# Kernel optimization log

Hardware: AMD Instinct MI355X
Metric: run time of the kernel (lower is better)

## Reference

```python
import math
import jax, jax.numpy as jnp
import numpy as np

NUM_HEADS = 16
NUM_LANDMARKS = 64
INV_ITERS = 6
ATT_SIZE = 1024
HEAD_SIZE = ATT_SIZE // NUM_HEADS  # dk = 64
NEG = -100000.0


def moore_penrose_pinv(x, num_iter):
    # lucidrains-style iterative Moore-Penrose pseudo-inverse
    abs_x = jnp.abs(x)
    col = abs_x.sum(axis=-1)
    row = abs_x.sum(axis=-2)
    z = jnp.swapaxes(x, -1, -2) / (jnp.max(col) * jnp.max(row))
    I = jnp.eye(x.shape[-1], dtype=x.dtype)
    for _ in range(num_iter):
        xz = x @ z
        z = 0.25 * z @ (13.0 * I - xz @ (15.0 * I - xz @ (7.0 * I - xz)))
    return z


def masked_softmax_scores(k, q, mask):
    # q @ k^T (dk=1: q already scaled) + mask, softmax over last dim
    s = jnp.einsum('bhmd,bhld->bhml', q, k)
    if mask is not None:
        s = s + (1.0 - mask) * NEG
    return jax.nn.softmax(s, axis=-1)


def setup_inputs() -> dict:
    key = jax.random.key(0)
    k1, k2, k3 = jax.random.split(key, 3)
    B, L, D = 4, 4096, 1024
    x = jax.random.normal(k1, (B, L, D), dtype=jnp.float32)
    attention_mask = jnp.ones((B, L), dtype=jnp.float32)
    w_kqv = jax.random.normal(k2, (3 * ATT_SIZE, D), dtype=jnp.float32) * 0.02
    w_out = jax.random.normal(k3, (ATT_SIZE, ATT_SIZE), dtype=jnp.float32) * 0.02
    b_out = jnp.zeros((ATT_SIZE,), dtype=jnp.float32)
    return {"x": x, "attention_mask": attention_mask,
            "w_kqv": w_kqv, "w_out": w_out, "b_out": b_out}


def reference(x, attention_mask, w_kqv, w_out, b_out):
    B, L, D = x.shape
    H, nl, hd = NUM_HEADS, NUM_LANDMARKS, HEAD_SIZE
    seg = L // nl  # landmark segment length (L already a multiple of nl)

    kqv = x @ w_kqv.T  # [B, L, 3A]
    k, q, v = jnp.split(kqv, 3, axis=-1)
    split = lambda t: t.reshape(B, L, H, hd).transpose(0, 2, 1, 3)  # [B,H,L,hd]
    k, q, v = split(k), split(q), split(v)

    mask = attention_mask[:, None, :]  # [B,1,L]
    denom = mask.reshape(B, 1, nl, seg).sum(-1) + 1e-08  # [B,1,nl]
    mask_lm = (denom > 0).astype(x.dtype)  # [B,1,nl]
    denom4 = denom[..., None]              # [B,1,nl,1]
    maskL = mask[..., None]                # [B,1,L,1]

    q = q * maskL
    k = k * maskL
    v = v * maskL

    s1_mask = maskL * mask_lm[..., None, :]               # [B,1,L,nl]
    s2_mask = mask_lm[..., None] * mask_lm[..., None, :]  # [B,1,nl,nl]
    s3_mask = jnp.swapaxes(s1_mask, -1, -2)               # [B,1,nl,L]

    q = q / math.sqrt(HEAD_SIZE)
    q_lm = q.reshape(B, H, nl, seg, hd).sum(-2) / denom4  # [B,H,nl,hd]
    k_lm = k.reshape(B, H, nl, seg, hd).sum(-2) / denom4

    scores_1 = masked_softmax_scores(k_lm, q, s1_mask)     # [B,H,L,nl]
    scores_2 = masked_softmax_scores(k_lm, q_lm, s2_mask)  # [B,H,nl,nl]
    scores_3 = masked_softmax_scores(k, q_lm, s3_mask)     # [B,H,nl,L]

    z_star = moore_penrose_pinv(scores_2, INV_ITERS)       # [B,H,nl,nl]
    out = scores_1 @ (z_star @ (scores_3 @ v))             # [B,H,L,hd]

    out = out.transpose(0, 2, 1, 3).reshape(B, L, H * hd)  # merge heads
    return out @ w_out.T + b_out
```

## Files before the change

kernel.cpp:

```cpp
#include <hip/hip_runtime.h>
#include <hip/hip_bf16.h>


static constexpr int Bn  = 4;
static constexpr int Ln  = 4096;
static constexpr int Dn  = 1024;
static constexpr int Hn  = 16;
static constexpr int HDn = 64;
static constexpr int NLn = 64;
static constexpr int SEGn = 64;
static constexpr int BHn = Bn * Hn;
static constexpr int Mn  = Bn * Ln;
static constexpr int NCH = 8;
#define NEG_BIG (-100000.0f)

static constexpr size_t OFF_KT  = 0;
static constexpr size_t OFF_QT  = 16777216;
static constexpr size_t OFF_VT  = 33554432;
static constexpr size_t OFF_WOH = 33554432;
static constexpr size_t OFF_WH  = 50331648;
static constexpr size_t OFF_QLM = 50331648;
static constexpr size_t OFF_KLM = 50593792;
static constexpr size_t OFF_S2  = 50855936;
static constexpr size_t OFF_Z   = 51118080;
static constexpr size_t OFF_WM  = 51380224;
static constexpr size_t OFF_PM  = 51642368;
static constexpr size_t OFF_PS  = 51675136;
static constexpr size_t OFF_GM  = 51707904;
static constexpr size_t OFF_XS  = 53477376;
static constexpr size_t OFF_PO  = 53477376;

using bf16x8 = __attribute__((ext_vector_type(8))) short;
using f32x16 = __attribute__((ext_vector_type(16))) float;
using s16x4  = __attribute__((ext_vector_type(4))) short;

__device__ __forceinline__ unsigned short f2bf(float f) {
    unsigned int u = __float_as_uint(f);
    return (unsigned short)((u + 0x7fffu + ((u >> 16) & 1u)) >> 16);
}
__device__ __forceinline__ void cvt8r(const float* fs, bf16x8& hv) {
    #pragma unroll
    for (int e = 0; e < 8; ++e) hv[e] = (short)f2bf(fs[e]);
}
typedef __attribute__((address_space(1))) void gvoid;
typedef __attribute__((address_space(3))) void lvoid;
__device__ __forceinline__ void async16(void* l, const void* g) {
    __builtin_amdgcn_global_load_lds((gvoid*)(size_t)g, (lvoid*)l, 16, 0, 0);
}

__global__ __launch_bounds__(256) void k_pack(
    const float* __restrict__ src, unsigned short* __restrict__ dh, int row0)
{
    __shared__ float Ls[128][33];
    const int rt = blockIdx.x, kt = blockIdx.y;
    const int tid = threadIdx.x;
    #pragma unroll
    for (int p = 0; p < 4; ++p) {
        const int row = p * 32 + (tid >> 3);
        const int c4 = (tid & 7) * 4;
        const float4 v = *(const float4*)&src[(size_t)(row0 + rt * 128 + row) * 1024 + kt * 32 + c4];
        Ls[row][c4 + 0] = v.x; Ls[row][c4 + 1] = v.y;
        Ls[row][c4 + 2] = v.z; Ls[row][c4 + 3] = v.w;
    }
    __syncthreads();
    const size_t tb = (size_t)(rt * 32 + kt) * 4096;
    for (int s = tid; s < 512; s += 256) {
        const int g = s >> 7, kk = (s >> 6) & 1, l = s & 63;
        const int row = g * 32 + (l & 31);
        const int k0 = kk * 16 + ((l >> 5) & 1) * 8;
        bf16x8 hv;
        cvt8r(&Ls[row][k0], hv);
        *(bf16x8*)&dh[tb + s * 8] = hv;
    }
}

#define GEMM4W_CORE(A_, B_, NNB)                                               \
    __shared__ __attribute__((aligned(16))) char smem[16384];                  \
    const int tid = threadIdx.x;                                               \
    const int lane = tid & 63, wid = tid >> 6;                                 \
    const int cpx = gridDim.x >> 3;                                            \
    const int wg = (blockIdx.x & 7) * cpx + (blockIdx.x >> 3);                 \
    const int bm = wg / (NNB), bn = wg % (NNB);                                \
    const int wrow = wid >> 1, wcol = wid & 1;                                 \
    const unsigned short* gsrc =                                               \
        (wid < 2 ? (A_) + (size_t)bm * 131072 : (B_) + (size_t)bn * 131072)    \
        + (wid & 1) * 2048 + lane * 8;                                         \
    char* ldst = smem + wid * 4096;                                            \
    f32x16 acc[2][2] = {};                                                     \
    for (int kt = 0; kt < 32; ++kt) {                                          \
        const unsigned short* g = gsrc + (size_t)kt * 4096;                    \
        __syncthreads();                                                       \
        _Pragma("unroll")                                                      \
        for (int i = 0; i < 4; ++i)                                            \
            async16(ldst + i * 1024, g + i * 512);                             \
        __syncthreads();                                                       \
        _Pragma("unroll")                                                      \
        for (int kk = 0; kk < 2; ++kk) {                                       \
            bf16x8 fa[2], fb[2];                                               \
            _Pragma("unroll")                                                  \
            for (int ti = 0; ti < 2; ++ti) {                                   \
                const int o = (((wrow * 2 + ti) * 2 + kk) << 10) + lane * 16;  \
                fa[ti] = *(const bf16x8*)(smem + o);                           \
            }                                                                  \
            _Pragma("unroll")                                                  \
            for (int tj = 0; tj < 2; ++tj) {                                   \
                const int o = (((wcol * 2 + tj) * 2 + kk) << 10) + lane * 16;  \
                fb[tj] = *(const bf16x8*)(smem + 8192 + o);                    \
            }                                                                  \
            _Pragma("unroll")                                                  \
            for (int ti = 0; ti < 2; ++ti)                                     \
                _Pragma("unroll")                                              \
                for (int tj = 0; tj < 2; ++tj)                                 \
                    acc[ti][tj] = __builtin_amdgcn_mfma_f32_32x32x16_bf16(     \
                        fa[ti], fb[tj], acc[ti][tj], 0, 0, 0);                 \
        }                                                                      \
    }

__global__ __launch_bounds__(256) void k_kqv_gemm(
    const unsigned short* __restrict__ xh,
    const unsigned short* __restrict__ wh,
    const float* __restrict__ mask,
    float* __restrict__ Kt, float* __restrict__ Qt, float* __restrict__ Vt,
    int row0)
{
    GEMM4W_CORE(xh, wh, 24)
    const int part = bn >> 3;
    #pragma unroll
    for (int ti = 0; ti < 2; ++ti) {
        #pragma unroll
        for (int tj = 0; tj < 2; ++tj) {
            const int col = (bn * 128 + wcol * 64 + tj * 32 + (lane & 31)) & 1023;
            const int h = col >> 6, d = col & 63;
            #pragma unroll
            for (int r = 0; r < 16; ++r) {
                const int row = row0 + bm * 128 + wrow * 64 + ti * 32
                              + (r & 3) + 8 * (r >> 2) + 4 * (lane >> 5);
                const int b = row >> 12, l = row & 4095;
                const float mk = mask[b * Ln + l];
                const size_t idx = ((size_t)(b * Hn + h) * Ln + l) * HDn + d;
                const float v = acc[ti][tj][r] * mk;
                if (part == 0)      Kt[idx] = v;
                else if (part == 1) Qt[idx] = v * 0.125f;
                else                Vt[idx] = v;
            }
        }
    }
}

__global__ __launch_bounds__(256) void k_out_gemm(
    const unsigned short* __restrict__ ah_,
    const unsigned short* __restrict__ bh_,
    const float* __restrict__ bias, float* __restrict__ out)
{
    GEMM4W_CORE(ah_, bh_, 8)
    #pragma unroll
    for (int ti = 0; ti < 2; ++ti) {
        #pragma unroll
        for (int tj = 0; tj < 2; ++tj) {
            const int col = bn * 128 + wcol * 64 + tj * 32 + (lane & 31);
            const float bb = bias[col];
            #pragma unroll
            for (int r = 0; r < 16; ++r) {
                const int row = bm * 128 + wrow * 64 + ti * 32
                              + (r & 3) + 8 * (r >> 2) + 4 * (lane >> 5);
                out[(size_t)row * Dn + col] = acc[ti][tj][r] + bb;
            }
        }
    }
}

__global__ __launch_bounds__(64) void k_landmarks(
    const float* __restrict__ Kt, const float* __restrict__ Qt,
    const float* __restrict__ mask,
    float* __restrict__ klm, float* __restrict__ qlm, int* __restrict__ gmax)
{
    const int blk = blockIdx.x;
    const int m = blk & 63, bh = blk >> 6, b = bh >> 4;
    const int d = threadIdx.x;
    if (blk == 0 && d < 2) gmax[d] = 0;
    float mv = mask[b * Ln + m * SEGn + d];
    #pragma unroll
    for (int off = 32; off; off >>= 1) mv += __shfl_down(mv, off);
    const float denom = __shfl(mv, 0) + 1e-8f;
    const float* kp = Kt + ((size_t)bh * Ln + m * SEGn) * HDn + d;
    const float* qp = Qt + ((size_t)bh * Ln + m * SEGn) * HDn + d;
    float sk = 0.f, sq = 0.f;
    for (int j = 0; j < SEGn; ++j) {
        sk += kp[(size_t)j * HDn];
        sq += qp[(size_t)j * HDn];
    }
    klm[((size_t)bh * NLn + m) * HDn + d] = sk / denom;
    qlm[((size_t)bh * NLn + m) * HDn + d] = sq / denom;
}

__global__ __launch_bounds__(256) void k_s2(
    const float* __restrict__ qlm, const float* __restrict__ klm,
    float* __restrict__ s2, int* __restrict__ gmax)
{
    const int bh = blockIdx.x;
    __shared__ float ql[64][65];
    __shared__ float kl[64][65];
    __shared__ float sr[64][65];
    __shared__ float red[64][4], red2[64][4];
    __shared__ float rtmp[64], ctmp[64];
    const int tid = threadIdx.x;
    for (int idx = tid; idx < 4096; idx += 256) {
        ql[idx >> 6][idx & 63] = qlm[(size_t)bh * 4096 + idx];
        kl[idx >> 6][idx & 63] = klm[(size_t)bh * 4096 + idx];
    }
    __syncthreads();
    const int row = tid >> 2, sg = tid & 3, c0 = sg * 16;
    float sv[16];
    float mx = -1e30f;
    #pragma unroll 4
    for (int m = 0; m < 16; ++m) {
        float s = 0.f;
        #pragma unroll 8
        for (int d2 = 0; d2 < 64; ++d2) s = fmaf(ql[row][d2], kl[c0 + m][d2], s);
        sv[m] = s;
        mx = fmaxf(mx, s);
    }
    red[row][sg] = mx;
    __syncthreads();
    mx = fmaxf(fmaxf(red[row][0], red[row][1]), fmaxf(red[row][2], red[row][3]));
    float sum = 0.f;
    #pragma unroll
    for (int m = 0; m < 16; ++m) {
        const float e = __expf(sv[m] - mx);
        sv[m] = e;
        sum += e;
    }
    red2[row][sg] = sum;
    __syncthreads();
    const float inv = 1.f / (red2[row][0] + red2[row][1] + red2[row][2] + red2[row][3]);
    float rs = 0.f;
    #pragma unroll
    for (int m = 0; m < 16; ++m) {
        const float v = sv[m] * inv;
        sr[row][c0 + m] = v;
        s2[(size_t)bh * 4096 + row * 64 + c0 + m] = v;
        rs += fabsf(v);
    }
    red[row][sg] = rs;
    __syncthreads();
    if (sg == 0)
        rtmp[row] = red[row][0] + red[row][1] + red[row][2] + red[row][3];
    float cs = 0.f;
    #pragma unroll
    for (int r = 0; r < 16; ++r) cs += fabsf(sr[c0 + r][row]);
    red2[row][sg] = cs;
    __syncthreads();
    if (sg == 0)
        ctmp[row] = red2[row][0] + red2[row][1] + red2[row][2] + red2[row][3];
    __syncthreads();
    if (tid < 64) {
        float rmax = rtmp[tid], cmax = ctmp[tid];
        #pragma unroll
        for (int off = 32; off; off >>= 1) {
            rmax = fmaxf(rmax, __shfl_down(rmax, off));
            cmax = fmaxf(cmax, __shfl_down(cmax, off));
        }
        if (tid == 0) {
            atomicMax(&gmax[0], __float_as_int(rmax));
            atomicMax(&gmax[1], __float_as_int(cmax));
        }
    }
}

template<int SUB>
__device__ __forceinline__ void mm64v(
    float* C, int ldc, const float* Ag, int lda,
    const float* Bm, int ldb, float dg, float scl)
{
    const int tid = threadIdx.x;
    const int tx = tid & 15, ty = tid >> 4;
    const int i0 = ty << 2, j0 = tx << 2;
    float acc[4][4] = {};
    for (int k0 = 0; k0 < 64; k0 += 4) {
        float4 a4[4], b4[4];
        #pragma unroll
        for (int i = 0; i < 4; ++i)
            a4[i] = *(const float4*)&Ag[(size_t)(i0 + i) * lda + k0];
        #pragma unroll
        for (int kk = 0; kk < 4; ++kk)
            b4[kk] = *(const float4*)&Bm[(size_t)(k0 + kk) * ldb + j0];
        if (SUB) {
            #pragma unroll
            for (int kk = 0; kk < 4; ++kk) {
                float* bp = (float*)&b4[kk];
                #pragma unroll
                for (int j = 0; j < 4; ++j)
                    bp[j] = ((k0 + kk == j0 + j) ? dg : 0.0f) - bp[j];
            }
        }
        #pragma unroll
        for (int i = 0; i < 4; ++i) {
            const float* ap = (const float*)&a4[i];
            #pragma unroll
            for (int kk = 0; kk < 4; ++kk) {
                const float* bp = (const float*)&b4[kk];
                #pragma unroll
                for (int j = 0; j < 4; ++j)
                    acc[i][j] = fmaf(ap[kk], bp[j], acc[i][j]);
            }
        }
    }
    __syncthreads();
    #pragma unroll
    for (int i = 0; i < 4; ++i)
        #pragma unroll
        for (int j = 0; j < 4; ++j) C[(size_t)(i0 + i) * ldc + j0 + j] = scl * acc[i][j];
    __syncthreads();
}

__global__ __launch_bounds__(256) void k_pinv_s3v(
    const float* __restrict__ s2, const int* __restrict__ gmax,
    float* __restrict__ zout,
    const float* __restrict__ qlm, const float* __restrict__ Kt,
    const float* __restrict__ Vt, const float* __restrict__ mask,
    float* __restrict__ Opart, float* __restrict__ mpart, float* __restrict__ spart)
{
    __shared__ __attribute__((aligned(16))) char shm[61184];
    const int tid = threadIdx.x;

    if (blockIdx.y == NCH) {
        float (*Zb)[68] = (float(*)[68])(shm);
        float (*XZ)[68] = (float(*)[68])(shm + 17408);
        float (*Tb)[68] = (float(*)[68])(shm + 34816);
        const int bh = blockIdx.x;
        const float* X = s2 + (size_t)bh * 4096;
        const float scale = 1.0f / (__int_as_float(gmax[0]) * __int_as_float(gmax[1]));
        for (int idx = tid; idx < 4096; idx += 256) {
            const int i = idx >> 6, j = idx & 63;
            Zb[i][j] = X[j * 64 + i] * scale;
        }
        __syncthreads();
        for (int it = 0; it < 6; ++it) {
            mm64v<0>(&XZ[0][0], 68, X, 64, &Zb[0][0], 68, 0.f, 1.f);
            mm64v<1>(&Tb[0][0], 68, &XZ[0][0], 68, &XZ[0][0], 68, 7.f, 1.f);
            mm64v<1>(&Tb[0][0], 68, &XZ[0][0], 68, &Tb[0][0], 68, 15.f, 1.f);
            mm64v<1>(&Zb[0][0], 68, &Zb[0][0], 68, &Tb[0][0], 68, 13.f, 0.25f);
        }
        for (int idx = tid; idx < 4096; idx += 256)
            zout[(size_t)bh * 4096 + idx] = Zb[idx >> 6][idx & 63];
        return;
    }

    float (*Sm)[65] = (float(*)[65])(shm);
    float (*Ks)[65] = (float(*)[65])(shm + 16640);
    float (*Vs)[65] = (float(*)[65])(shm + 33280);
    unsigned short* Qp = (unsigned short*)(shm + 49920);
    float (*red)[4]  = (float(*)[4])(shm + 58112);
    float (*red2)[4] = (float(*)[4])(shm + 59136);
    float* rowmax = (float*)(shm + 60160);
    float* rowsum = (float*)(shm + 60416);
    float* fac    = (float*)(shm + 60672);
    float* mrow   = (float*)(shm + 60928);
    const int bh = blockIdx.x, ch = blockIdx.y;
    const int b = bh >> 4;
    const int lane = tid & 63, wid = tid >> 6;
    const int wr = wid >> 1, wc = wid & 1;

    for (int idx = tid; idx < 4096; idx += 256)
        Sm[idx >> 6][idx & 63] = qlm[(size_t)bh * 4096 + idx];
    if (tid < 64) { rowmax[tid] = -1e30f; rowsum[tid] = 0.f; }
    __syncthreads();
    for (int s = tid; s < 512; s += 256) {
        const int g = s >> 8, kc = (s >> 6) & 3, l = s & 63;
        const int row = g * 32 + (l & 31);
        const int k0 = kc * 16 + ((l >> 5) & 1) * 8;
        bf16x8 hv;
        cvt8r(&Sm[row][k0], hv);
        *(bf16x8*)&Qp[s * 8] = hv;
    }
    f32x16 accO = {};
    const int t0beg = ch * (Ln / NCH), t0end = t0beg + (Ln / NCH);
    for (int t0 = t0beg; t0 < t0end; t0 += 64) {
        __syncthreads();
        for (int idx = tid; idx < 4096; idx += 256) {
            const int r = idx >> 6, c2 = idx & 63;
            Ks[r][c2] = Kt[((size_t)bh * Ln + t0 + r) * HDn + c2];
            Vs[r][c2] = Vt[((size_t)bh * Ln + t0 + r) * HDn + c2];
        }
        if (tid < 64) mrow[tid] = mask[b * Ln + t0 + tid];
        __syncthreads();
        f32x16 acc = {};
        #pragma unroll
        for (int kc = 0; kc < 4; ++kc) {
            const bf16x8 a_h = *(const bf16x8*)&Qp[((wr * 4 + kc) * 64 + lane) * 8];
            const int brow = wc * 32 + (lane & 31);
            const int k0 = kc * 16 + (lane >> 5) * 8;
            bf16x8 b_h;
            cvt8r(&Ks[brow][k0], b_h);
            acc = __builtin_amdgcn_mfma_f32_32x32x16_bf16(a_h, b_h, acc, 0, 0, 0);
        }
        #pragma unroll
        for (int r = 0; r < 16; ++r) {
            const int row = wr * 32 + (r & 3) + 8 * (r >> 2) + 4 * (lane >> 5);
            const int col = wc * 32 + (lane & 31);
            Sm[row][col] = acc[r] + (1.f - mrow[col]) * NEG_BIG;
        }
        __syncthreads();
        {
            const int row = tid >> 2, sg = tid & 3, c0 = sg * 16;
            float mx = -1e30f;
            #pragma unroll
            for (int c = 0; c < 16; ++c) mx = fmaxf(mx, Sm[row][c0 + c]);
            red[row][sg] = mx;
            __syncthreads();
            const float nm = fmaxf(rowmax[row],
                fmaxf(fmaxf(red[row][0], red[row][1]), fmaxf(red[row][2], red[row][3])));
            const float f = __expf(rowmax[row] - nm);
            float ps = 0.f;
            #pragma unroll
            for (int c = 0; c < 16; ++c) {
                const float e = __expf(Sm[row][c0 + c] - nm);
                Sm[row][c0 + c] = e;
                ps += e;
            }
            red2[row][sg] = ps;
            __syncthreads();
            if (sg == 0) {
                rowsum[row] = rowsum[row] * f
                    + red2[row][0] + red2[row][1] + red2[row][2] + red2[row][3];
                rowmax[row] = nm;
                fac[row] = f;
            }
        }
        __syncthreads();
        #pragma unroll
        for (int r = 0; r < 16; ++r) {
            const int row = wr * 32 + (r & 3) + 8 * (r >> 2) + 4 * (lane >> 5);
            accO[r] *= fac[row];
        }
        #pragma unroll
        for (int kc = 0; kc < 4; ++kc) {
            const int arow = wr * 32 + (lane & 31);
            const int ak0 = kc * 16 + (lane >> 5) * 8;
            bf16x8 a_h;
            cvt8r(&Sm[arow][ak0], a_h);
            const int bcol = wc * 32 + (lane & 31);
            const int bk0 = kc * 16 + (lane >> 5) * 8;
            float bw[8];
            #pragma unroll
            for (int e = 0; e < 8; ++e) bw[e] = Vs[bk0 + e][bcol];
            bf16x8 b_h;
            cvt8r(bw, b_h);
            accO = __builtin_amdgcn_mfma_f32_32x32x16_bf16(a_h, b_h, accO, 0, 0, 0);
        }
    }
    __syncthreads();
    #pragma unroll
    for (int r = 0; r < 16; ++r) {
        const int row = wr * 32 + (r & 3) + 8 * (r >> 2) + 4 * (lane >> 5);
        Vs[row][wc * 32 + (lane & 31)] = accO[r];
    }
    __syncthreads();
    const size_t ob = (size_t)(bh * NCH + ch) * 4096;
    for (int idx = tid; idx < 4096; idx += 256)
        Opart[ob + idx] = Vs[idx >> 6][idx & 63];
    if (tid < 64) {
        mpart[(bh * NCH + ch) * 64 + tid] = rowmax[tid];
        spart[(bh * NCH + ch) * 64 + tid] = rowsum[tid];
    }
}

__global__ __launch_bounds__(256) void k_mergez(
    const float* __restrict__ Opart, const float* __restrict__ mpart,
    const float* __restrict__ spart, const float* __restrict__ Zs,
    float* __restrict__ Wm)
{
    __shared__ float Sv[64][68];
    __shared__ float Zb[64][68];
    const int bh = blockIdx.x, tid = threadIdx.x;
    for (int idx = tid; idx < 4096; idx += 256)
        Zb[idx >> 6][idx & 63] = Zs[(size_t)bh * 4096 + idx];
    {
        const int r = tid >> 2, c0 = (tid & 3) * 16;
        float e[NCH];
        float M = -1e30f;
        #pragma unroll
        for (int c = 0; c < NCH; ++c) {
            e[c] = mpart[(bh * NCH + c) * 64 + r];
            M = fmaxf(M, e[c]);
        }
        float S = 0.f;
        #pragma unroll
        for (int c = 0; c < NCH; ++c) {
            e[c] = expf(e[c] - M);
            S += spart[(bh * NCH + c) * 64 + r] * e[c];
        }
        const float invS = 1.f / S;
        for (int col = c0; col < c0 + 16; ++col) {
            float o = 0.f;
            #pragma unroll
            for (int c = 0; c < NCH; ++c)
                o += Opart[(size_t)(bh * NCH + c) * 4096 + r * 64 + col] * e[c];
            Sv[r][col] = o * invS;
        }
    }
    __syncthreads();
    const int tx = tid & 15, ty = tid >> 4;
    const int i0 = ty << 2, j0 = tx << 2;
    float acc[4][4] = {};
    for (int k0 = 0; k0 < 64; k0 += 4) {
        float4 a4[4], b4[4];
        #pragma unroll
        for (int i = 0; i < 4; ++i)
            a4[i] = *(const float4*)&Zb[i0 + i][k0];
        #pragma unroll
        for (int kk = 0; kk < 4; ++kk)
            b4[kk] = *(const float4*)&Sv[k0 + kk][j0];
        #pragma unroll
        for (int i = 0; i < 4; ++i) {
            const float* ap = (const float*)&a4[i];
            #pragma unroll
            for (int kk = 0; kk < 4; ++kk) {
                const float* bp = (const float*)&b4[kk];
                #pragma unroll
                for (int j = 0; j < 4; ++j)
                    acc[i][j] = fmaf(ap[kk], bp[j], acc[i][j]);
            }
        }
    }
    #pragma unroll
    for (int i = 0; i < 4; ++i)
        #pragma unroll
        for (int j = 0; j < 4; ++j)
            Wm[(size_t)bh * 4096 + (i0 + i) * 64 + j0 + j] = acc[i][j];
}

__global__ __launch_bounds__(256) void k_attn_out(
    const float* __restrict__ Qt, const float* __restrict__ klm,
    const float* __restrict__ Wm, unsigned short* __restrict__ ah)
{
    const int lt0 = blockIdx.x * 4;
    const int bh = blockIdx.y;
    const int b = bh >> 4, h = bh & 15;
    __shared__ float Sm[64][65];
    __shared__ float Ks[64][65];
    __shared__ float Ws[64][65];
    __shared__ float Ob[64][65];
    __shared__ unsigned short Qp[4096];
    __shared__ float red[64][4], red2[64][4];
    __shared__ float invr[64];
    const int tid = threadIdx.x;
    const int lane = tid & 63, wid = tid >> 6;
    const int wr = wid >> 1, wc = wid & 1;

    for (int idx = tid; idx < 4096; idx += 256) {
        const int r = idx >> 6, c2 = idx & 63;
        Ks[r][c2] = klm[(size_t)bh * 4096 + idx];
        Ws[r][c2] = Wm[(size_t)bh * 4096 + idx];
    }
    __syncthreads();

    for (int sub = 0; sub < 4; ++sub) {
        const int lt = lt0 + sub;
        for (int idx = tid; idx < 4096; idx += 256)
            Sm[idx >> 6][idx & 63] = Qt[((size_t)bh * Ln + lt * 64 + (idx >> 6)) * HDn + (idx & 63)];
        __syncthreads();
        for (int s = tid; s < 512; s += 256) {
            const int g = s >> 8, kc = (s >> 6) & 3, l = s & 63;
            const int row = g * 32 + (l & 31);
            const int k0 = kc * 16 + ((l >> 5) & 1) * 8;
            bf16x8 hv;
            cvt8r(&Sm[row][k0], hv);
            *(bf16x8*)&Qp[s * 8] = hv;
        }
        __syncthreads();
        f32x16 acc = {};
        #pragma unroll
        for (int kc = 0; kc < 4; ++kc) {
            const bf16x8 a_h = *(const bf16x8*)&Qp[((wr * 4 + kc) * 64 + lane) * 8];
            const int brow = wc * 32 + (lane & 31);
            const int k0 = kc * 16 + (lane >> 5) * 8;
            bf16x8 b_h;
            cvt8r(&Ks[brow][k0], b_h);
            acc = __builtin_amdgcn_mfma_f32_32x32x16_bf16(a_h, b_h, acc, 0, 0, 0);
        }
        #pragma unroll
        for (int r = 0; r < 16; ++r) {
            const int row = wr * 32 + (r & 3) + 8 * (r >> 2) + 4 * (lane >> 5);
            Sm[row][wc * 32 + (lane & 31)] = acc[r];
        }
        __syncthreads();
        {
            const int row = tid >> 2, sg = tid & 3, c0 = sg * 16;
            float mx = -1e30f;
            #pragma unroll
            for (int c = 0; c < 16; ++c) mx = fmaxf(mx, Sm[row][c0 + c]);
            red[row][sg] = mx;
            __syncthreads();
            mx = fmaxf(fmaxf(red[row][0], red[row][1]), fmaxf(red[row][2], red[row][3]));
            float ps = 0.f;
            #pragma unroll
            for (int c = 0; c < 16; ++c) {
                const float e = __expf(Sm[row][c0 + c] - mx);
                Sm[row][c0 + c] = e;
                ps += e;
            }
            red2[row][sg] = ps;
            __syncthreads();
            if (sg == 0)
                invr[row] = 1.f / (red2[row][0] + red2[row][1] + red2[row][2] + red2[row][3]);
        }
        __syncthreads();
        f32x16 acc2 = {};
        #pragma unroll
        for (int kc = 0; kc < 4; ++kc) {
            const int arow = wr * 32 + (lane & 31);
            const int ak0 = kc * 16 + (lane >> 5) * 8;
            bf16x8 a_h;
            cvt8r(&Sm[arow][ak0], a_h);
            const int bcol = wc * 32 + (lane & 31);
            const int bk0 = kc * 16 + (lane >> 5) * 8;
            float bw[8];
            #pragma unroll
            for (int e = 0; e < 8; ++e) bw[e] = Ws[bk0 + e][bcol];
            bf16x8 b_h;
            cvt8r(bw, b_h);
            acc2 = __builtin_amdgcn_mfma_f32_32x32x16_bf16(a_h, b_h, acc2, 0, 0, 0);
        }
        __syncthreads();
        #pragma unroll
        for (int r = 0; r < 16; ++r) {
            const int row = wr * 32 + (r & 3) + 8 * (r >> 2) + 4 * (lane >> 5);
            Ob[row][wc * 32 + (lane & 31)] = acc2[r];
        }
        __syncthreads();
        {
            const int tx = tid & 15, ty = tid >> 4;
            const int i0 = ty << 2, j0 = tx << 2;
            const int kd = h * 64 + j0;
            const int kt2 = kd >> 5, kc2 = kd & 31;
            const int kk2 = kc2 >> 4, half = (kc2 & 15) >> 3, e0 = kc2 & 7;
            #pragma unroll
            for (int i = 0; i < 4; ++i) {
                const float inv = invr[i0 + i];
                const int gm = b * Ln + lt * 64 + i0 + i;
                const int mt = gm >> 7, g2 = (gm & 127) >> 5, lrow = gm & 31;
                const size_t u = (size_t)(mt * 32 + kt2) * 4096
                               + (size_t)(((g2 * 2 + kk2) * 64 + half * 32 + lrow) * 8 + e0);
                s16x4 hv;
                #pragma unroll
                for (int j = 0; j < 4; ++j)
                    hv[j] = (short)f2bf(Ob[i0 + i][j0 + j] * inv);
                *(s16x4*)&ah[u] = hv;
            }
        }
        __syncthreads();
    }
}

extern "C" void kernel_launch(void* const* d_in, const int* in_sizes, int n_in,
                              void* d_out, int out_size, void* d_ws, size_t ws_size,
                              hipStream_t stream)
{
    (void)in_sizes; (void)n_in; (void)out_size;
    const float* x    = (const float*)d_in[0];
    const float* mask = (const float*)d_in[1];
    const float* wkqv = (const float*)d_in[2];
    const float* wout = (const float*)d_in[3];
    const float* bout = (const float*)d_in[4];
    float* out = (float*)d_out;
    float* ws  = (float*)d_ws;

    float* Kt   = ws + OFF_KT;
    float* Qt   = ws + OFF_QT;
    float* Vt   = ws + OFF_VT;
    float* qlm  = ws + OFF_QLM;
    float* klm  = ws + OFF_KLM;
    float* s2   = ws + OFF_S2;
    float* zst  = ws + OFF_Z;
    float* Wm   = ws + OFF_WM;
    int*   gmax = (int*)(ws + OFF_GM);
    float* mpart = ws + OFF_PM;
    float* spart = ws + OFF_PS;
    float* Opart = ws + OFF_PO;
    unsigned short* wh  = (unsigned short*)(ws + OFF_WH);
    unsigned short* woh = (unsigned short*)(ws + OFF_WOH);
    unsigned short* attn_h = (unsigned short*)(ws + OFF_KT);

    int S = 2048;
    if (ws_size >= (size_t)(OFF_XS + 16384 * 512) * 4) S = 16384;
    else if (ws_size >= (size_t)(OFF_XS + 8192 * 512) * 4) S = 8192;
    else if (ws_size >= (size_t)(OFF_XS + 2097152) * 4) S = 4096;
    unsigned short* xhs = (unsigned short*)(ws + OFF_XS);

    k_pack<<<dim3(24, 32), 256, 0, stream>>>(wkqv, wh, 0);
    for (int s = 0; s < Mn / S; ++s) {
        k_pack<<<dim3(S / 128, 32), 256, 0, stream>>>(x, xhs, s * S);
        k_kqv_gemm<<<(S / 128) * 24, 256, 0, stream>>>(
            xhs, wh, mask, Kt, Qt, Vt, s * S);
    }
    k_landmarks<<<BHn * NLn, 64, 0, stream>>>(Kt, Qt, mask, klm, qlm, gmax);
    k_s2<<<BHn, 256, 0, stream>>>(qlm, klm, s2, gmax);
    k_pinv_s3v<<<dim3(BHn, NCH + 1), 256, 0, stream>>>(
        s2, gmax, zst, qlm, Kt, Vt, mask, Opart, mpart, spart);
    k_pack<<<dim3(8, 32), 256, 0, stream>>>(wout, woh, 0);
    k_mergez<<<BHn, 256, 0, stream>>>(Opart, mpart, spart, zst, Wm);
    k_attn_out<<<dim3(Ln / 256, BHn), 256, 0, stream>>>(Qt, klm, Wm, attn_h);
    k_out_gemm<<<128 * 8, 256, 0, stream>>>(attn_h, woh, bout, out);
}
```

Baseline: 402.5 us.

## Double-buffer LDS tiles in GEMM core with async prefetch two stages ahead

Splits the shared-memory staging buffer of the 4-wave GEMM core into two halves. The async global-to-LDS loads for chunks c+1 and c+2 are issued while chunk c is being computed, with explicit vmcnt waits and raw s_barrier calls replacing the two __syncthreads per iteration. The goal is to hide global load latency behind the MFMA work in the QKV and output projection GEMMs. In exchange it doubles LDS use per block, which may reduce occupancy, and the hand-written waitcnt logic depends on each wave having exactly four outstanding loads per chunk.

```diff
diff --git a/kernel.cpp b/kernel.cpp
--- a/kernel.cpp
+++ b/kernel.cpp
@@ -75,7 +75,7 @@
 }
 
 #define GEMM4W_CORE(A_, B_, NNB)                                               \
-    __shared__ __attribute__((aligned(16))) char smem[16384];                  \
+    __shared__ __attribute__((aligned(16))) char smem[2][16384];               \
     const int tid = threadIdx.x;                                               \
     const int lane = tid & 63, wid = tid >> 6;                                 \
     const int cpx = gridDim.x >> 3;                                            \
@@ -85,34 +85,47 @@
     const unsigned short* gsrc =                                               \
         (wid < 2 ? (A_) + (size_t)bm * 131072 : (B_) + (size_t)bn * 131072)    \
         + (wid & 1) * 2048 + lane * 8;                                         \
-    char* ldst = smem + wid * 4096;                                            \
     f32x16 acc[2][2] = {};                                                     \
-    for (int kt = 0; kt < 32; ++kt) {                                          \
-        const unsigned short* g = gsrc + (size_t)kt * 4096;                    \
-        __syncthreads();                                                       \
-        _Pragma("unroll")                                                      \
-        for (int i = 0; i < 4; ++i)                                            \
-            async16(ldst + i * 1024, g + i * 512);                             \
-        __syncthreads();                                                       \
-        _Pragma("unroll")                                                      \
-        for (int kk = 0; kk < 2; ++kk) {                                       \
-            bf16x8 fa[2], fb[2];                                               \
+    {                                                                          \
+        auto ISSUE = [&](int c, int b) {                                       \
+            const unsigned short* g = gsrc + (size_t)c * 4096;                 \
+            char* l = smem[b] + wid * 4096;                                    \
             _Pragma("unroll")                                                  \
-            for (int ti = 0; ti < 2; ++ti) {                                   \
-                const int o = (((wrow * 2 + ti) * 2 + kk) << 10) + lane * 16;  \
-                fa[ti] = *(const bf16x8*)(smem + o);                           \
+            for (int i = 0; i < 4; ++i)                                        \
+                async16(l + i * 1024, g + i * 512);                            \
+        };                                                                     \
+        ISSUE(0, 0);                                                           \
+        ISSUE(1, 1);                                                           \
+        _Pragma("unroll 1")                                                    \
+        for (int c = 0; c < 32; ++c) {                                         \
+            if (c < 31) asm volatile("s_waitcnt vmcnt(4)" ::: "memory");       \
+            else        asm volatile("s_waitcnt vmcnt(0)" ::: "memory");       \
+            __builtin_amdgcn_s_barrier();                                      \
+            __builtin_amdgcn_sched_barrier(0);                                 \
+            const char* sb = (const char*)smem[c & 1];                         \
+            _Pragma("unroll")                                                  \
+            for (int kk = 0; kk < 2; ++kk) {                                   \
+                bf16x8 fa[2], fb[2];                                           \
+                _Pragma("unroll")                                              \
+                for (int ti = 0; ti < 2; ++ti) {                               \
+                    const int o = (((wrow * 2 + ti) * 2 + kk) << 10) + lane * 16; \
+                    fa[ti] = *(const bf16x8*)(sb + o);                         \
+                }                                                              \
+                _Pragma("unroll")                                              \
+                for (int tj = 0; tj < 2; ++tj) {                               \
+                    const int o = (((wcol * 2 + tj) * 2 + kk) << 10) + lane * 16; \
+                    fb[tj] = *(const bf16x8*)(sb + 8192 + o);                  \
+                }                                                              \
+                _Pragma("unroll")                                              \
+                for (int ti = 0; ti < 2; ++ti)                                 \
+                    _Pragma("unroll")                                          \
+                    for (int tj = 0; tj < 2; ++tj)                             \
+                        acc[ti][tj] = __builtin_amdgcn_mfma_f32_32x32x16_bf16( \
+                            fa[ti], fb[tj], acc[ti][tj], 0, 0, 0);             \
             }                                                                  \
-            _Pragma("unroll")                                                  \
-            for (int tj = 0; tj < 2; ++tj) {                                   \
-                const int o = (((wcol * 2 + tj) * 2 + kk) << 10) + lane * 16;  \
-                fb[tj] = *(const bf16x8*)(smem + 8192 + o);                    \
-            }                                                                  \
-            _Pragma("unroll")                                                  \
-            for (int ti = 0; ti < 2; ++ti)                                     \
-                _Pragma("unroll")                                              \
-                for (int tj = 0; tj < 2; ++tj)                                 \
-                    acc[ti][tj] = __builtin_amdgcn_mfma_f32_32x32x16_bf16(     \
-                        fa[ti], fb[tj], acc[ti][tj], 0, 0, 0);                 \
+            __builtin_amdgcn_sched_barrier(0);                                 \
+            __builtin_amdgcn_s_barrier();                                      \
+            if (c + 2 < 32) ISSUE(c + 2, c & 1);                               \
         }                                                                      \
     }
 
```

Result: no change. 401.9 us (-0.1%).
